# Performance work log

Hardware: AMD Instinct MI355X
Metric: run time of the kernel (lower is better)

## Reference

```python
import jax, jax.numpy as jnp
import numpy as np

N = 50000      # nodes
E = 800000     # edges
IN = 128       # in_dim
H = 8          # heads
C = 16         # h_dim (per-head out channels)
ED = 16        # edge_dim
G = 1000       # number of graphs
HC = H * C     # 128
EPS = 1e-16    # PyG softmax epsilon


def setup_inputs() -> dict:
    key = jax.random.key(0)
    ks = jax.random.split(key, 32)
    p = lambda i, shape: jax.random.normal(ks[i], shape, jnp.float32) * 0.1
    inp = {
        "x": jax.random.normal(ks[0], (N, IN), jnp.float32),
        "edge_index": jax.random.randint(ks[1], (2, E), 0, N),
        "edge_attr": jax.random.normal(ks[2], (E, ED), jnp.float32),
        "batch": jnp.sort(jax.random.randint(ks[3], (N,), 0, G)),
    }
    dims = [IN, HC, HC]
    for l in range(3):
        d = dims[l]
        inp[f"W{l+1}"] = p(4 + 6 * l, (d, HC))     # lin weight
        inp[f"We{l+1}"] = p(5 + 6 * l, (ED, HC))   # lin_edge weight
        inp[f"as{l+1}"] = p(6 + 6 * l, (H, C))     # att_src
        inp[f"ad{l+1}"] = p(7 + 6 * l, (H, C))     # att_dst
        inp[f"ae{l+1}"] = p(8 + 6 * l, (H, C))     # att_edge
        inp[f"b{l+1}"] = jnp.zeros((HC,), jnp.float32)
    D = 4 * HC  # cat(h1,h2,h3,h_pool_) -> 512
    inp["Wl1"] = p(22, (D, D)); inp["bl1"] = jnp.zeros((D,), jnp.float32)
    inp["Wl2"] = p(23, (D, 1)); inp["bl2"] = jnp.zeros((1,), jnp.float32)
    return inp


def gat_conv(x, src, dst, edge_attr, W, We, a_s, a_d, a_e, b):
    # x: [N, d_in] -> xs: [N, H, C]
    xs = (x @ W).reshape(-1, H, C)
    ea = (edge_attr @ We).reshape(-1, H, C)          # [E, H, C]
    al_src = jnp.sum(xs * a_s, axis=-1)              # [N, H]
    al_dst = jnp.sum(xs * a_d, axis=-1)              # [N, H]
    al_e = jnp.sum(ea * a_e, axis=-1)                # [E, H]
    alpha = al_src[src] + al_dst[dst] + al_e         # [E, H]
    alpha = jax.nn.leaky_relu(alpha, 0.2)
    amax = jax.ops.segment_max(alpha, dst, num_segments=N)
    ex = jnp.exp(alpha - amax[dst])
    denom = jax.ops.segment_sum(ex, dst, num_segments=N)
    alpha = ex / (denom[dst] + EPS)                  # softmax over in-edges of dst
    msg = xs[src] * alpha[..., None]                 # [E, H, C]
    out = jax.ops.segment_sum(msg, dst, num_segments=N)  # [N, H, C]
    return out.reshape(-1, HC) + b


def reference(x, edge_index, edge_attr, batch,
              W1, We1, as1, ad1, ae1, b1,
              W2, We2, as2, ad2, ae2, b2,
              W3, We3, as3, ad3, ae3, b3,
              Wl1, bl1, Wl2, bl2):
    src, dst = edge_index[0], edge_index[1]
    h1 = gat_conv(x, src, dst, edge_attr, W1, We1, as1, ad1, ae1, b1)
    h2 = gat_conv(h1, src, dst, edge_attr, W2, We2, as2, ad2, ae2, b2)
    h3 = gat_conv(h2, src, dst, edge_attr, W3, We3, as3, ad3, ae3, b3)
    # global_add_pool then broadcast back per node (vectorized gather,
    # replacing the original per-node python loop)
    h_pool = jax.ops.segment_sum(h3, batch, num_segments=G)   # [G, HC]
    h_pool_ = h_pool[batch]                                    # [N, HC]
    h = jnp.concatenate([h1, h2, h3, h_pool_], axis=1)         # [N, 4*HC]
    h = jax.nn.leaky_relu(h @ Wl1 + bl1, 0.01)
    return h @ Wl2 + bl2
```

## Files before the change

kernel.cpp:

```cpp
#include <hip/hip_runtime.h>

#define N_NODES 50000
#define N_EDGES 800000
#define N_GRAPH 1000

typedef short bf16x8 __attribute__((ext_vector_type(8)));
typedef float f32x4 __attribute__((ext_vector_type(4)));

__device__ inline short f2b(float f) {
    union { float f; unsigned u; } x; x.f = f;
    unsigned r = x.u + 0x7FFF + ((x.u >> 16) & 1);
    return (short)(r >> 16);
}
__device__ inline float b2f_lo(unsigned v) {
    union { unsigned u; float f; } x; x.u = v << 16; return x.f;
}
__device__ inline float b2f_hi(unsigned v) {
    union { unsigned u; float f; } x; x.u = v & 0xFFFF0000u; return x.f;
}
__device__ inline float b2f_s(short s) {
    union { unsigned u; float f; } x; x.u = ((unsigned)(unsigned short)s) << 16; return x.f;
}
__device__ inline unsigned pack2(short lo, short hi) {
    return ((unsigned)(unsigned short)lo) | (((unsigned)(unsigned short)hi) << 16);
}

__global__ void f2b_bulk(const float* __restrict__ in, short* __restrict__ out, int n4) {
    int t = blockIdx.x * blockDim.x + threadIdx.x;
    if (t >= n4) return;
    float4 v = *(const float4*)(in + (size_t)t * 4);
    *(short4*)(out + (size_t)t * 4) = make_short4(f2b(v.x), f2b(v.y), f2b(v.z), f2b(v.w));
}

__global__ void wbt_k(const float* __restrict__ W, short* __restrict__ WbT) {
    int idx = blockIdx.x * blockDim.x + threadIdx.x;
    int k = idx >> 7, c = idx & 127;
    WbT[(size_t)c * 128 + k] = f2b(W[idx]);
}

__global__ __launch_bounds__(256) void gemm_mfma(const short* __restrict__ Ab,
                                                 const short* __restrict__ WbT,
                                                 float* __restrict__ out,
                                                 short* __restrict__ outb, int nrows) {
    const int tid = threadIdx.x;
    const int n0 = blockIdx.x * 64;
    const int wid = tid >> 6, lane = tid & 63;
    const int lr = lane & 15, kg = lane >> 4;
    const int wr = (wid >> 1) * 32;
    const int wc = (wid & 1) * 64;

    f32x4 acc[2][4] = {};

#pragma unroll
    for (int ks = 0; ks < 4; ks++) {
        const int k0 = ks * 32;
        bf16x8 a[2], b[4];
#pragma unroll
        for (int fm = 0; fm < 2; fm++) {
            int gr = n0 + wr + fm * 16 + lr;
            bf16x8 v = {};
            if (gr < nrows) v = *(const bf16x8*)(Ab + (size_t)gr * 128 + k0 + kg * 8);
            a[fm] = v;
        }
#pragma unroll
        for (int fn = 0; fn < 4; fn++)
            b[fn] = *(const bf16x8*)(WbT + (size_t)(wc + fn * 16 + lr) * 128 + k0 + kg * 8);
#pragma unroll
        for (int fm = 0; fm < 2; fm++)
#pragma unroll
            for (int fn = 0; fn < 4; fn++)
                acc[fm][fn] = __builtin_amdgcn_mfma_f32_16x16x32_bf16(
                    a[fm], b[fn], acc[fm][fn], 0, 0, 0);
    }
#pragma unroll
    for (int fm = 0; fm < 2; fm++) {
#pragma unroll
        for (int r = 0; r < 4; r++) {
            int gr = n0 + wr + fm * 16 + kg * 4 + r;
            if (gr < nrows) {
#pragma unroll
                for (int fn = 0; fn < 4; fn++) {
                    int col = wc + fn * 16 + lr;
                    float z = acc[fm][fn][r];
                    out[(size_t)gr * 128 + col] = z;
                    outb[(size_t)gr * 128 + col] = f2b(z);
                }
            }
        }
    }
}

__global__ void node_al(const float* __restrict__ xs, const float* __restrict__ a_s,
                        const float* __restrict__ a_d, float* __restrict__ alsrc,
                        float* __restrict__ aldst, int n) {
    int t = blockIdx.x * blockDim.x + threadIdx.x;
    if (t >= n * 8) return;
    int node = t >> 3, h = t & 7;
    const float4* xp = (const float4*)(xs + (size_t)node * 128 + h * 16);
    const float4* sp = (const float4*)(a_s + h * 16);
    const float4* dp = (const float4*)(a_d + h * 16);
    float ss = 0.f, dd = 0.f;
#pragma unroll
    for (int q = 0; q < 4; q++) {
        float4 x4 = xp[q], s4 = sp[q], d4 = dp[q];
        ss += x4.x * s4.x + x4.y * s4.y + x4.z * s4.z + x4.w * s4.w;
        dd += x4.x * d4.x + x4.y * d4.y + x4.z * d4.z + x4.w * d4.w;
    }
    alsrc[t] = ss;
    aldst[t] = dd;
}

__global__ void aew_k(const float* __restrict__ We, const float* __restrict__ ae,
                      float* __restrict__ aeW) {
    int t = threadIdx.x;
    int k = t >> 3, h = t & 7;
    float s = 0.f;
#pragma unroll
    for (int c = 0; c < 16; c++) s += We[k * 128 + h * 16 + c] * ae[h * 16 + c];
    aeW[k * 8 + h] = s;
}

__global__ void hist_k(const int* __restrict__ ei, int* __restrict__ cnt, int ne) {
    int e = blockIdx.x * blockDim.x + threadIdx.x;
    if (e < ne) atomicAdd(&cnt[ei[ne + e]], 1);
}

__global__ void scan1_k(const int* __restrict__ cnt, int* __restrict__ rowptr,
                        int* __restrict__ part, int n) {
    __shared__ int s[256];
    int tid = threadIdx.x;
    int i = blockIdx.x * 256 + tid;
    int v = (i < n) ? cnt[i] : 0;
    s[tid] = v; __syncthreads();
#pragma unroll
    for (int off = 1; off < 256; off <<= 1) {
        int t = (tid >= off) ? s[tid - off] : 0;
        __syncthreads();
        s[tid] += t;
        __syncthreads();
    }
    if (i < n) rowptr[i] = s[tid] - v;
    if (tid == 255) part[blockIdx.x] = s[255];
}

__global__ void scan2_k(int* __restrict__ part, int npart) {
    __shared__ int s[256];
    int tid = threadIdx.x;
    int v = (tid < npart) ? part[tid] : 0;
    s[tid] = v; __syncthreads();
#pragma unroll
    for (int off = 1; off < 256; off <<= 1) {
        int t = (tid >= off) ? s[tid - off] : 0;
        __syncthreads();
        s[tid] += t;
        __syncthreads();
    }
    if (tid < npart) part[tid] = s[tid] - v;
}

__global__ void scan3_k(int* __restrict__ rowptr, const int* __restrict__ part,
                        int* __restrict__ cursor, int n, int ne) {
    int i = blockIdx.x * 256 + threadIdx.x;
    if (i < n) {
        int r = rowptr[i] + part[blockIdx.x];
        rowptr[i] = r;
        cursor[i] = r;
    }
    if (i == 0) rowptr[n] = ne;
}

__global__ void scatter_k(const int* __restrict__ ei, int* __restrict__ cursor,
                          int* __restrict__ pos, int* __restrict__ csr_src, int ne) {
    int e = blockIdx.x * blockDim.x + threadIdx.x;
    if (e >= ne) return;
    int d = ei[ne + e];
    int p = atomicAdd(&cursor[d], 1);
    pos[e] = p;
    csr_src[p] = ei[e];
}

__global__ __launch_bounds__(256) void ale_k(const int* __restrict__ ei,
                                             const float* __restrict__ eattr,
                                             const float* __restrict__ alsrc,
                                             const float* __restrict__ aeW,
                                             const int* __restrict__ pos,
                                             short* __restrict__ aleb, int ne) {
    __shared__ float sAe[128];
    if (threadIdx.x < 128) sAe[threadIdx.x] = aeW[threadIdx.x];
    __syncthreads();
    int e = blockIdx.x * blockDim.x + threadIdx.x;
    if (e >= ne) return;
    float ea[16];
    const float4* ep = (const float4*)(eattr + (size_t)e * 16);
#pragma unroll
    for (int q = 0; q < 4; q++) {
        float4 v = ep[q];
        ea[q * 4 + 0] = v.x; ea[q * 4 + 1] = v.y; ea[q * 4 + 2] = v.z; ea[q * 4 + 3] = v.w;
    }
    int s = ei[e];
    float out[8];
#pragma unroll
    for (int h = 0; h < 8; h++) out[h] = alsrc[s * 8 + h];
#pragma unroll
    for (int k = 0; k < 16; k++)
#pragma unroll
        for (int h = 0; h < 8; h++) out[h] += ea[k] * sAe[k * 8 + h];
    short v8[8];
#pragma unroll
    for (int h = 0; h < 8; h++) v8[h] = f2b(out[h]);
    short* op = aleb + (size_t)pos[e] * 8;
    *(short4*)(op)     = make_short4(v8[0], v8[1], v8[2], v8[3]);
    *(short4*)(op + 4) = make_short4(v8[4], v8[5], v8[6], v8[7]);
}

__global__ __launch_bounds__(256) void gather_k(const int* __restrict__ rowptr,
                                                const int* __restrict__ csr_src,
                                                const short* __restrict__ aleb,
                                                const float* __restrict__ aldst,
                                                const short* __restrict__ xsb,
                                                const float* __restrict__ b,
                                                short* __restrict__ houtb, int n) {
    int dst = blockIdx.x * 4 + (threadIdx.x >> 6);
    if (dst >= n) return;
    const int lane = threadIdx.x & 63;
    const int h = lane >> 3;
    const float L2E = 1.44269504f;
    int p0 = rowptr[dst], p1 = rowptr[dst + 1];
    float ald = aldst[dst * 8 + h];
    float den = 0.f, acc0 = 0.f, acc1 = 0.f;
    int p = p0;
    for (; p + 8 <= p1; p += 8) {
        int   sv  = csr_src[p + (lane & 7)];
        float alv = b2f_s(aleb[(size_t)p * 8 + lane]);
        int s0 = __shfl(sv, 0), s1 = __shfl(sv, 1), s2 = __shfl(sv, 2), s3 = __shfl(sv, 3);
        int s4 = __shfl(sv, 4), s5 = __shfl(sv, 5), s6 = __shfl(sv, 6), s7 = __shfl(sv, 7);
        unsigned v0 = *(const unsigned*)(xsb + (size_t)s0 * 128 + lane * 2);
        unsigned v1 = *(const unsigned*)(xsb + (size_t)s1 * 128 + lane * 2);
        unsigned v2 = *(const unsigned*)(xsb + (size_t)s2 * 128 + lane * 2);
        unsigned v3 = *(const unsigned*)(xsb + (size_t)s3 * 128 + lane * 2);
        unsigned v4 = *(const unsigned*)(xsb + (size_t)s4 * 128 + lane * 2);
        unsigned v5 = *(const unsigned*)(xsb + (size_t)s5 * 128 + lane * 2);
        unsigned v6 = *(const unsigned*)(xsb + (size_t)s6 * 128 + lane * 2);
        unsigned v7 = *(const unsigned*)(xsb + (size_t)s7 * 128 + lane * 2);
        unsigned vv[8] = {v0, v1, v2, v3, v4, v5, v6, v7};
#pragma unroll
        for (int i = 0; i < 8; i++) {
            float al = __shfl(alv, i * 8 + h);
            float lg = al + ald; lg = lg > 0.f ? lg : 0.2f * lg;
            float ex = exp2f(lg * L2E);
            den  += ex;
            acc0 += b2f_lo(vv[i]) * ex;
            acc1 += b2f_hi(vv[i]) * ex;
        }
    }
    for (; p + 1 < p1; p += 2) {
        int s0 = csr_src[p];
        int s1 = csr_src[p + 1];
        float al0 = b2f_s(aleb[(size_t)p * 8 + h]);
        float al1 = b2f_s(aleb[(size_t)(p + 1) * 8 + h]);
        unsigned v0 = *(const unsigned*)(xsb + (size_t)s0 * 128 + lane * 2);
        unsigned v1 = *(const unsigned*)(xsb + (size_t)s1 * 128 + lane * 2);
        float lg0 = al0 + ald; lg0 = lg0 > 0.f ? lg0 : 0.2f * lg0;
        float lg1 = al1 + ald; lg1 = lg1 > 0.f ? lg1 : 0.2f * lg1;
        float ex0 = exp2f(lg0 * L2E);
        float ex1 = exp2f(lg1 * L2E);
        den  += ex0 + ex1;
        acc0 += b2f_lo(v0) * ex0 + b2f_lo(v1) * ex1;
        acc1 += b2f_hi(v0) * ex0 + b2f_hi(v1) * ex1;
    }
    if (p < p1) {
        int s0 = csr_src[p];
        float al0 = b2f_s(aleb[(size_t)p * 8 + h]);
        unsigned v0 = *(const unsigned*)(xsb + (size_t)s0 * 128 + lane * 2);
        float lg0 = al0 + ald; lg0 = lg0 > 0.f ? lg0 : 0.2f * lg0;
        float ex0 = exp2f(lg0 * L2E);
        den  += ex0;
        acc0 += b2f_lo(v0) * ex0;
        acc1 += b2f_hi(v0) * ex0;
    }
    float inv = 1.f / (den + 1e-16f);
    const float2 bb = *(const float2*)(b + lane * 2);
    unsigned o = pack2(f2b(acc0 * inv + bb.x), f2b(acc1 * inv + bb.y));
    *(unsigned*)(houtb + (size_t)dst * 128 + lane * 2) = o;
}

__global__ void pool_k(const short* __restrict__ h3b, const int* __restrict__ batch,
                       float* __restrict__ pool, int n) {
    int t = blockIdx.x * blockDim.x + threadIdx.x;
    if (t >= n * 128) return;
    int node = t >> 7, j = t & 127;
    atomicAdd(pool + (size_t)batch[node] * 128 + j, b2f_s(h3b[t]));
}

__global__ void wl1t_k(const float* __restrict__ Wl1, short* __restrict__ Wl1T) {
    int idx = blockIdx.x * blockDim.x + threadIdx.x;
    int k = idx >> 9, c = idx & 511;
    Wl1T[(size_t)c * 512 + k] = f2b(Wl1[idx]);
}

__global__ void init_out(float* __restrict__ out, const float* __restrict__ bl2, int n) {
    int t = blockIdx.x * blockDim.x + threadIdx.x;
    if (t < n) out[t] = bl2[0];
}

__global__ __launch_bounds__(256) void final_mfma(
    const short* __restrict__ h1, const short* __restrict__ h2,
    const short* __restrict__ h3, const short* __restrict__ poolb,
    const int* __restrict__ batch, const short* __restrict__ Wl1T,
    const float* __restrict__ bl1, const float* __restrict__ Wl2,
    float* __restrict__ out, int nrows)
{
    __shared__ short Abuf[4 * 64 * 8];
    __shared__ int   sBatch[64];
    const int tid = threadIdx.x;
    const int n0 = blockIdx.x * 64;
    const int j0 = blockIdx.y * 256;
    const int wid = tid >> 6, lane = tid & 63;
    const int lr = lane & 15, kg = lane >> 4;

    if (tid < 64) {
        int gr = n0 + tid;
        sBatch[tid] = (gr < nrows) ? batch[gr] : 0;
    }
    __syncthreads();

    f32x4 acc[4][4] = {};

    for (int k0 = 0; k0 < 512; k0 += 32) {
        const int seg = k0 >> 7;
        const short* base = (seg == 0) ? h1 : (seg == 1) ? h2 : (seg == 2) ? h3 : poolb;
        const int cseg = k0 & 127;
        {
            int gr = n0 + lane;
            int grow = (seg == 3) ? sBatch[lane] : ((gr < nrows) ? gr : 0);
            const short* src = base + (size_t)grow * 128 + cseg + wid * 8;
#if __has_builtin(__builtin_amdgcn_global_load_lds)
            __builtin_amdgcn_global_load_lds(
                (const __attribute__((address_space(1))) unsigned int*)src,
                (__attribute__((address_space(3))) unsigned int*)&Abuf[(wid * 64 + lane) * 8],
                16, 0, 0);
#else
            uint4 v = *(const uint4*)src;
            *(uint4*)(&Abuf[(wid * 64 + lane) * 8]) = v;
#endif
        }
        __syncthreads();
        bf16x8 a[4], b[4];
#pragma unroll
        for (int fm = 0; fm < 4; fm++)
            a[fm] = *(const bf16x8*)(&Abuf[(kg * 64 + fm * 16 + lr) * 8]);
#pragma unroll
        for (int fn = 0; fn < 4; fn++)
            b[fn] = *(const bf16x8*)(Wl1T + (size_t)(j0 + wid * 64 + fn * 16 + lr) * 512
                                     + k0 + kg * 8);
#pragma unroll
        for (int fm = 0; fm < 4; fm++)
#pragma unroll
            for (int fn = 0; fn < 4; fn++)
                acc[fm][fn] = __builtin_amdgcn_mfma_f32_16x16x32_bf16(
                    a[fm], b[fn], acc[fm][fn], 0, 0, 0);
        __syncthreads();
    }

    float w2[4], b1c[4];
#pragma unroll
    for (int fn = 0; fn < 4; fn++) {
        int c = j0 + wid * 64 + fn * 16 + lr;
        w2[fn]  = Wl2[c];
        b1c[fn] = bl1[c];
    }

#pragma unroll
    for (int fm = 0; fm < 4; fm++) {
#pragma unroll
        for (int r = 0; r < 4; r++) {
            float s = 0.f;
#pragma unroll
            for (int fn = 0; fn < 4; fn++) {
                float z = acc[fm][fn][r] + b1c[fn];
                z = z > 0.f ? z : 0.01f * z;
                s += z * w2[fn];
            }
            s += __shfl_xor(s, 1);
            s += __shfl_xor(s, 2);
            s += __shfl_xor(s, 4);
            s += __shfl_xor(s, 8);
            if (lr == 0) {
                int gr = n0 + fm * 16 + kg * 4 + r;
                if (gr < nrows) atomicAdd(out + gr, s);
            }
        }
    }
}

extern "C" void kernel_launch(void* const* d_in, const int* in_sizes, int n_in,
                              void* d_out, int out_size, void* d_ws, size_t ws_size,
                              hipStream_t stream) {
    const float* x     = (const float*)d_in[0];
    const int*   ei    = (const int*)d_in[1];
    const float* eattr = (const float*)d_in[2];
    const int*   batch = (const int*)d_in[3];
    const float* W[3]   = {(const float*)d_in[4],  (const float*)d_in[10], (const float*)d_in[16]};
    const float* We[3]  = {(const float*)d_in[5],  (const float*)d_in[11], (const float*)d_in[17]};
    const float* as_[3] = {(const float*)d_in[6],  (const float*)d_in[12], (const float*)d_in[18]};
    const float* ad_[3] = {(const float*)d_in[7],  (const float*)d_in[13], (const float*)d_in[19]};
    const float* ae_[3] = {(const float*)d_in[8],  (const float*)d_in[14], (const float*)d_in[20]};
    const float* b_[3]  = {(const float*)d_in[9],  (const float*)d_in[15], (const float*)d_in[21]};
    const float* Wl1 = (const float*)d_in[22];
    const float* bl1 = (const float*)d_in[23];
    const float* Wl2 = (const float*)d_in[24];
    const float* bl2 = (const float*)d_in[25];

    const int N = N_NODES, E = N_EDGES, G = N_GRAPH;

    float* ws    = (float*)d_ws;
    float* xs    = ws;
    float* alsrc = xs + (size_t)N * 128;
    float* aldst = alsrc + (size_t)N * 8;
    float* pool  = aldst + (size_t)N * 8;
    float* aeW   = pool + (size_t)G * 128;
    short* xb    = (short*)(aeW + 128);
    short* xsb   = xb + (size_t)N * 128;
    short* hb0   = xsb + (size_t)N * 128;
    short* hb1   = hb0 + (size_t)N * 128;
    short* hb2   = hb1 + (size_t)N * 128;
    short* hb[3] = {hb0, hb1, hb2};
    short* poolb = hb2 + (size_t)N * 128;
    short* wbt0  = poolb + (size_t)G * 128;
    short* wbt1  = wbt0 + 16384;
    short* wbt2  = wbt1 + 16384;
    short* wbt[3] = {wbt0, wbt1, wbt2};
    short* wl1t  = wbt2 + 16384;
    short* aleb  = wl1t + 262144;
    int*   cnt     = (int*)(aleb + (size_t)E * 8);
    int*   rowptr  = cnt + N;
    int*   cursor  = rowptr + N + 1;
    int*   part    = cursor + N;
    int*   pos     = part + 256;
    int*   csr_src = pos + E;

    f2b_bulk<<<(N * 32 + 255) / 256, 256, 0, stream>>>(x, xb, N * 32);
    for (int l = 0; l < 3; l++)
        wbt_k<<<64, 256, 0, stream>>>(W[l], wbt[l]);
    wl1t_k<<<1024, 256, 0, stream>>>(Wl1, wl1t);
    hipMemsetAsync(cnt, 0, (size_t)N * sizeof(int), stream);
    hist_k<<<(E + 255) / 256, 256, 0, stream>>>(ei, cnt, E);
    const int nblk = (N + 255) / 256;
    scan1_k<<<nblk, 256, 0, stream>>>(cnt, rowptr, part, N);
    scan2_k<<<1, 256, 0, stream>>>(part, nblk);
    scan3_k<<<nblk, 256, 0, stream>>>(rowptr, part, cursor, N, E);
    scatter_k<<<(E + 255) / 256, 256, 0, stream>>>(ei, cursor, pos, csr_src, E);

    for (int l = 0; l < 3; l++) {
        const short* Ain = (l == 0) ? xb : hb[l - 1];
        gemm_mfma<<<(N + 63) / 64, 256, 0, stream>>>(Ain, wbt[l], xs, xsb, N);
        node_al<<<(N * 8 + 255) / 256, 256, 0, stream>>>(xs, as_[l], ad_[l], alsrc, aldst, N);
        aew_k<<<1, 128, 0, stream>>>(We[l], ae_[l], aeW);
        ale_k<<<(E + 255) / 256, 256, 0, stream>>>(ei, eattr, alsrc, aeW, pos, aleb, E);
        gather_k<<<(N + 3) / 4, 256, 0, stream>>>(rowptr, csr_src, aleb, aldst, xsb,
                                                  b_[l], hb[l], N);
    }
    hipMemsetAsync(pool, 0, (size_t)G * 128 * sizeof(float), stream);
    pool_k<<<(N * 128 + 255) / 256, 256, 0, stream>>>(hb[2], batch, pool, N);
    f2b_bulk<<<(G * 32 + 255) / 256, 256, 0, stream>>>(pool, poolb, G * 32);

    init_out<<<(N + 255) / 256, 256, 0, stream>>>((float*)d_out, bl2, N);
    dim3 fg((N + 63) / 64, 2);
    final_mfma<<<fg, 256, 0, stream>>>(hb[0], hb[1], hb[2], poolb, batch,
                                       wl1t, bl1, Wl2, (float*)d_out, N);
}
```

Baseline: 493.2 us.

## Double-buffer LDS A tiles and prefetch B fragments in final MFMA GEMM

The final dense layer kernel now double-buffers the A-tile LDS staging and prefetches the next K-step's Wl1T fragments into registers while the MFMAs for the current step run. One barrier per iteration is removed and global-load latency is meant to overlap with compute. The cost is twice the LDS for A and extra registers for the prefetched B fragments, which may lower occupancy. The K loop is also fully unrolled.

```diff
diff --git a/kernel.cpp b/kernel.cpp
--- a/kernel.cpp
+++ b/kernel.cpp
@@ -310,7 +310,7 @@
     const float* __restrict__ bl1, const float* __restrict__ Wl2,
     float* __restrict__ out, int nrows)
 {
-    __shared__ short Abuf[4 * 64 * 8];
+    __shared__ short Abuf[2][4 * 64 * 8];
     __shared__ int   sBatch[64];
     const int tid = threadIdx.x;
     const int n0 = blockIdx.x * 64;
@@ -324,42 +324,61 @@
     }
     __syncthreads();
 
+    const short* seg_base[4] = {h1, h2, h3, poolb};
+
+    auto STAGE = [&](int t) {
+        const int k0 = t * 32;
+        const int seg = k0 >> 7;
+        const short* base = seg_base[seg];
+        const int cseg = k0 & 127;
+        int gr = n0 + lane;
+        int grow = (seg == 3) ? sBatch[lane] : ((gr < nrows) ? gr : 0);
+        const short* src = base + (size_t)grow * 128 + cseg + wid * 8;
+#if __has_builtin(__builtin_amdgcn_global_load_lds)
+        __builtin_amdgcn_global_load_lds(
+            (const __attribute__((address_space(1))) unsigned int*)src,
+            (__attribute__((address_space(3))) unsigned int*)&Abuf[t & 1][(wid * 64 + lane) * 8],
+            16, 0, 0);
+#else
+        uint4 v = *(const uint4*)src;
+        *(uint4*)(&Abuf[t & 1][(wid * 64 + lane) * 8]) = v;
+#endif
+    };
+    auto LOADB = [&](int t, bf16x8* bb) {
+        const int k0 = t * 32;
+#pragma unroll
+        for (int fn = 0; fn < 4; fn++)
+            bb[fn] = *(const bf16x8*)(Wl1T + (size_t)(j0 + wid * 64 + fn * 16 + lr) * 512
+                                      + k0 + kg * 8);
+    };
+
     f32x4 acc[4][4] = {};
-
-    for (int k0 = 0; k0 < 512; k0 += 32) {
-        const int seg = k0 >> 7;
-        const short* base = (seg == 0) ? h1 : (seg == 1) ? h2 : (seg == 2) ? h3 : poolb;
-        const int cseg = k0 & 127;
-        {
-            int gr = n0 + lane;
-            int grow = (seg == 3) ? sBatch[lane] : ((gr < nrows) ? gr : 0);
-            const short* src = base + (size_t)grow * 128 + cseg + wid * 8;
-#if __has_builtin(__builtin_amdgcn_global_load_lds)
-            __builtin_amdgcn_global_load_lds(
-                (const __attribute__((address_space(1))) unsigned int*)src,
-                (__attribute__((address_space(3))) unsigned int*)&Abuf[(wid * 64 + lane) * 8],
-                16, 0, 0);
-#else
-            uint4 v = *(const uint4*)src;
-            *(uint4*)(&Abuf[(wid * 64 + lane) * 8]) = v;
-#endif
-        }
-        __syncthreads();
-        bf16x8 a[4], b[4];
+    bf16x8 bc[4], bn[4];
+
+    STAGE(0);
+    LOADB(0, bc);
+    __syncthreads();
+#pragma unroll
+    for (int t = 0; t < 16; t++) {
+        if (t < 15) {
+            STAGE(t + 1);
+            LOADB(t + 1, bn);
+        }
+        bf16x8 a[4];
 #pragma unroll
         for (int fm = 0; fm < 4; fm++)
-            a[fm] = *(const bf16x8*)(&Abuf[(kg * 64 + fm * 16 + lr) * 8]);
-#pragma unroll
-        for (int fn = 0; fn < 4; fn++)
-            b[fn] = *(const bf16x8*)(Wl1T + (size_t)(j0 + wid * 64 + fn * 16 + lr) * 512
-                                     + k0 + kg * 8);
+            a[fm] = *(const bf16x8*)(&Abuf[t & 1][(kg * 64 + fm * 16 + lr) * 8]);
 #pragma unroll
         for (int fm = 0; fm < 4; fm++)
 #pragma unroll
             for (int fn = 0; fn < 4; fn++)
                 acc[fm][fn] = __builtin_amdgcn_mfma_f32_16x16x32_bf16(
-                    a[fm], b[fn], acc[fm][fn], 0, 0, 0);
-        __syncthreads();
+                    a[fm], bc[fn], acc[fm][fn], 0, 0, 0);
+        if (t < 15) {
+            __syncthreads();
+#pragma unroll
+            for (int fn = 0; fn < 4; fn++) bc[fn] = bn[fn];
+        }
     }
 
     float w2[4], b1c[4];
```

Measured after the change: 487.6 us. No clear change (-1.1%).
